# Kernel tuning notes

Measured on AMD Instinct MI355X. Metric: run time of the kernel, lower is better.

The kernel has to match this reference:

```python
import jax, jax.numpy as jnp
import numpy as np

TEMPERATURE = 0.5


def setup_inputs() -> dict:
    key = jax.random.key(0)
    k1, k2 = jax.random.split(key)
    N, D = 8192, 128
    features = jax.random.normal(k1, (N, D), dtype=jnp.float32)
    labels = jax.random.randint(k2, (N,), 0, 10, dtype=jnp.int64)
    return {"features": features, "labels": labels}


def reference(features, labels):
    # cosine similarity via normalized matmul (fused form of the broadcasted version)
    eps = 1e-8
    norm = jnp.maximum(jnp.linalg.norm(features, axis=-1, keepdims=True), eps)
    fn = features / norm
    sim = jnp.einsum('id,jd->ij', fn, fn) / TEMPERATURE  # [N, N]

    pos_mask = labels[:, None] == labels[None, :]        # [N, N] bool
    pos_f = pos_mask.astype(sim.dtype)
    neg_f = 1.0 - pos_f

    exp_pos = jnp.exp(sim * pos_f)                       # [N, N]
    exp_neg = jnp.sum(jnp.exp(sim * neg_f), axis=1, keepdims=True)  # [N, 1]

    loss_mat = -jnp.log(exp_pos / (exp_pos + exp_neg))   # [N, N]
    # mean over positive entries (jit-safe masked mean)
    num_pos = jnp.sum(pos_f)
    loss = jnp.sum(loss_mat * pos_f) / num_pos
    return loss
```

## Files before the change

kernel.cpp:

```cpp
#include <hip/hip_runtime.h>
#include <hip/hip_bf16.h>
#include <math.h>

#define NROWS 8192
#define DIM 128
#define BM 128
#define BN 128
#define CS 8
#define COLS_PER_SLAB (NROWS / CS)
#define CT_ITERS (COLS_PER_SLAB / BN)
#define RS (NROWS / BM)
#define SCALE 1.69864368f
#define LN2F 0.69314718056f

typedef __attribute__((ext_vector_type(8))) short bf16x8;
typedef __attribute__((ext_vector_type(4))) float f32x4;

__device__ __forceinline__ void gload16(const void* g, void* l) {
  __builtin_amdgcn_global_load_lds(
      (const __attribute__((address_space(1))) void*)g,
      (__attribute__((address_space(3))) void*)l, 16, 0, 0);
}

__device__ __forceinline__ void stage_tile(const ushort* __restrict__ fnb, int row0,
                                           char* tile, int w, int lane) {
  const char* gb = reinterpret_cast<const char*>(fnb);
#pragma unroll
  for (int i = 0; i < 8; ++i) {
    int rl = w * 32 + i * 4 + (lane >> 4);
    int src = ((lane & 15) ^ (rl & 7)) << 4;
    gload16(gb + (size_t)(row0 + rl) * 256 + src, tile + w * 8192 + i * 1024);
  }
}

__global__ __launch_bounds__(256) void k_norm(const float* __restrict__ f,
                                              __hip_bfloat16* __restrict__ fnb,
                                              float* __restrict__ losssum) {
  if (blockIdx.x == 0 && threadIdx.x == 0) losssum[0] = 0.f;
  int wave = threadIdx.x >> 6;
  int lane = threadIdx.x & 63;
  int row = blockIdx.x * 4 + wave;
  const float* src = f + (size_t)row * DIM;
  float v0 = src[lane];
  float v1 = src[lane + 64];
  float ss = v0 * v0 + v1 * v1;
#pragma unroll
  for (int o = 32; o > 0; o >>= 1) ss += __shfl_down(ss, o);
  ss = __shfl(ss, 0);
  float inv = SCALE / fmaxf(sqrtf(ss), 1e-8f);
  __hip_bfloat16* dst = fnb + (size_t)row * DIM;
  dst[lane] = __float2bfloat16(v0 * inv);
  dst[lane + 64] = __float2bfloat16(v1 * inv);
}

__global__ __launch_bounds__(256, 2) void k_main(
    const ushort* __restrict__ fnb, const int* __restrict__ lab,
    float* __restrict__ P) {
  __shared__ char lds[2 * BM * 256];
  const int t = threadIdx.x;
  const int lane = t & 63;
  const int w = t >> 6;
  const int wm = w >> 1, wn = w & 1;
  const int g = lane >> 4, li16 = lane & 15;
  const int cs = blockIdx.x;
  const int i0 = blockIdx.y * BM;
  const int jslab = cs * COLS_PER_SLAB;

  stage_tile(fnb, i0, lds, w, lane);
  stage_tile(fnb, jslab, lds + 32768, w, lane);
  asm volatile("s_waitcnt vmcnt(8)" ::: "memory");
  __builtin_amdgcn_s_barrier();

  bf16x8 af[4][4];
#pragma unroll
  for (int m = 0; m < 4; ++m) {
    int r = wm * 64 + m * 16 + li16;
#pragma unroll
    for (int ks = 0; ks < 4; ++ks) {
      int cb = ((ks * 4 + g) ^ (r & 7)) << 4;
      af[m][ks] = *reinterpret_cast<const bf16x8*>(lds + r * 256 + cb);
    }
  }
  asm volatile("s_waitcnt lgkmcnt(0)" ::: "memory");
  __builtin_amdgcn_sched_barrier(0);
  __builtin_amdgcn_s_barrier();

  int lr[4][4];
#pragma unroll
  for (int m = 0; m < 4; ++m)
#pragma unroll
    for (int r = 0; r < 4; ++r)
      lr[m][r] = lab[i0 + wm * 64 + m * 16 + g * 4 + r];

  float a_tot[4][4] = {}, a_pos[4][4] = {}, a_sim[4][4] = {};

#pragma unroll 1
  for (int ct = 0; ct < CT_ITERS; ++ct) {
    const int j0 = jslab + ct * BN;
    char* bufc = lds + ((size_t)((ct & 1) ^ 1) << 15);
    if (ct < CT_ITERS - 1)
      stage_tile(fnb, j0 + BN, lds + ((size_t)(ct & 1) << 15), w, lane);

    f32x4 acc[4][4];
#pragma unroll
    for (int m = 0; m < 4; ++m)
#pragma unroll
      for (int n = 0; n < 4; ++n) acc[m][n] = (f32x4){0.f, 0.f, 0.f, 0.f};

#pragma unroll
    for (int ks = 0; ks < 4; ++ks) {
      bf16x8 bf[4];
#pragma unroll
      for (int n = 0; n < 4; ++n) {
        int r = wn * 64 + n * 16 + li16;
        int cb = ((ks * 4 + g) ^ (r & 7)) << 4;
        bf[n] = *reinterpret_cast<const bf16x8*>(bufc + r * 256 + cb);
      }
#pragma unroll
      for (int m = 0; m < 4; ++m)
#pragma unroll
        for (int n = 0; n < 4; ++n)
          acc[m][n] = __builtin_amdgcn_mfma_f32_16x16x32_bf16(af[m][ks], bf[n], acc[m][n], 0, 0, 0);
    }

#pragma unroll
    for (int n = 0; n < 4; ++n) {
      const int lc = lab[j0 + wn * 64 + n * 16 + li16];
#pragma unroll
      for (int m = 0; m < 4; ++m)
#pragma unroll
        for (int r = 0; r < 4; ++r) {
          float u = acc[m][n][r];
          float E = __builtin_exp2f(u);
          float msk = (lr[m][r] == lc) ? 1.f : 0.f;
          a_tot[m][r] += E;
          a_pos[m][r] = fmaf(msk, E, a_pos[m][r]);
          a_sim[m][r] = fmaf(msk, u, a_sim[m][r]);
        }
    }

    asm volatile("s_waitcnt vmcnt(0)" ::: "memory");
    __builtin_amdgcn_s_barrier();
  }

#pragma unroll
  for (int m = 0; m < 4; ++m)
#pragma unroll
    for (int r = 0; r < 4; ++r)
#pragma unroll
      for (int off = 8; off > 0; off >>= 1) {
        a_tot[m][r] += __shfl_xor(a_tot[m][r], off);
        a_pos[m][r] += __shfl_xor(a_pos[m][r], off);
        a_sim[m][r] += __shfl_xor(a_sim[m][r], off);
      }

  __syncthreads();
  float* red = reinterpret_cast<float*>(lds);
  if (li16 == 0) {
#pragma unroll
    for (int m = 0; m < 4; ++m)
#pragma unroll
      for (int r = 0; r < 4; ++r) {
        int rl = wm * 64 + m * 16 + g * 4 + r;
        red[(rl * 2 + wn) * 3 + 0] = a_tot[m][r];
        red[(rl * 2 + wn) * 3 + 1] = a_pos[m][r];
        red[(rl * 2 + wn) * 3 + 2] = a_sim[m][r];
      }
  }
  __syncthreads();
  if (wn == 0 && li16 == 0) {
#pragma unroll
    for (int m = 0; m < 4; ++m)
#pragma unroll
      for (int r = 0; r < 4; ++r) {
        int rl = wm * 64 + m * 16 + g * 4 + r;
        float* dst = P + ((size_t)cs * NROWS + (i0 + rl)) * 3;
        dst[0] = red[(rl * 2) * 3 + 0] + red[(rl * 2 + 1) * 3 + 0];
        dst[1] = red[(rl * 2) * 3 + 1] + red[(rl * 2 + 1) * 3 + 1];
        dst[2] = red[(rl * 2) * 3 + 2] + red[(rl * 2 + 1) * 3 + 2];
      }
  }
}

__global__ __launch_bounds__(1024) void k_rowfinal(
    const float* __restrict__ P, const int* __restrict__ lab,
    float* __restrict__ losssum) {
  __shared__ int sh[16][16];
  __shared__ int hist_s[16];
  __shared__ float sred[1024];
  const int t = threadIdx.x;
  const int w = t >> 6;
  if ((t & 63) < 16) sh[w][t & 63] = 0;
  __syncthreads();
#pragma unroll
  for (int it = 0; it < NROWS / 1024; ++it)
    atomicAdd(&sh[w][lab[t + it * 1024]], 1);
  __syncthreads();
  if (t < 16) {
    int s = 0;
#pragma unroll
    for (int x = 0; x < 16; ++x) s += sh[x][t];
    hist_s[t] = s;
  }
  __syncthreads();

  int i = blockIdx.x * 1024 + t;
  float st = 0.f, sp = 0.f, sa = 0.f;
#pragma unroll
  for (int cs = 0; cs < CS; ++cs) {
    const float* p = P + ((size_t)cs * NROWS + i) * 3;
    st += p[0]; sp += p[1]; sa += p[2];
  }
  float cnt = (float)hist_s[lab[i]];
  float negtot = st - sp + cnt;
  float li = cnt * logf(negtot) + sp / negtot - LN2F * sa;
  sred[t] = li;
  __syncthreads();
  for (int s2 = 512; s2 > 0; s2 >>= 1) {
    if (t < s2) sred[t] += sred[t + s2];
    __syncthreads();
  }
  if (t == 0) {
    atomicAdd(&losssum[0], sred[0]);
    if (blockIdx.x == 0) {
      int np = 0;
#pragma unroll
      for (int c = 0; c < 10; ++c) np += hist_s[c] * hist_s[c];
      losssum[1] = (float)np;
    }
  }
}

__global__ void k_out(const float* __restrict__ losssum, float* __restrict__ out) {
  if (threadIdx.x == 0) out[0] = losssum[0] / losssum[1];
}

extern "C" void kernel_launch(void* const* d_in, const int* in_sizes, int n_in,
                              void* d_out, int out_size, void* d_ws, size_t ws_size,
                              hipStream_t stream) {
  const float* feat = (const float*)d_in[0];
  const int* lab = (const int*)d_in[1];
  float* out = (float*)d_out;
  char* ws = (char*)d_ws;

  __hip_bfloat16* fnb = (__hip_bfloat16*)ws;
  size_t off = (size_t)NROWS * DIM * 2;
  float* P = (float*)(ws + off); off += (size_t)CS * NROWS * 3 * 4;
  float* losssum = (float*)(ws + off);

  k_norm<<<NROWS / 4, 256, 0, stream>>>(feat, fnb, losssum);
  k_main<<<dim3(CS, RS), 256, 0, stream>>>((const ushort*)fnb, lab, P);
  k_rowfinal<<<NROWS / 1024, 1024, 0, stream>>>(P, lab, losssum);
  k_out<<<1, 64, 0, stream>>>(losssum, out);
}
```

Measured before the change: 62.45 us.

## Single-buffer LDS tile, load A fragments directly, double column slabs

The number of column slabs doubles, so the grid gets twice as many blocks, each covering half as many column tiles. The LDS B tile changes from double-buffered to single-buffered with synchronous staging between iterations, halving LDS per block. A fragments now come straight from global memory instead of through LDS, and the min-blocks hint in launch_bounds is dropped. The aim is more parallelism and occupancy, but the load of each next tile no longer overlaps compute and the partials buffer and final reduction grow.

```diff
diff --git a/kernel.cpp b/kernel.cpp
--- a/kernel.cpp
+++ b/kernel.cpp
@@ -6,7 +6,7 @@
 #define DIM 128
 #define BM 128
 #define BN 128
-#define CS 8
+#define CS 16
 #define COLS_PER_SLAB (NROWS / CS)
 #define CT_ITERS (COLS_PER_SLAB / BN)
 #define RS (NROWS / BM)
@@ -53,10 +53,10 @@
   dst[lane + 64] = __float2bfloat16(v1 * inv);
 }
 
-__global__ __launch_bounds__(256, 2) void k_main(
+__global__ __launch_bounds__(256) void k_main(
     const ushort* __restrict__ fnb, const int* __restrict__ lab,
     float* __restrict__ P) {
-  __shared__ char lds[2 * BM * 256];
+  __shared__ char lds[BM * 256];
   const int t = threadIdx.x;
   const int lane = t & 63;
   const int w = t >> 6;
@@ -66,24 +66,16 @@
   const int i0 = blockIdx.y * BM;
   const int jslab = cs * COLS_PER_SLAB;
 
-  stage_tile(fnb, i0, lds, w, lane);
-  stage_tile(fnb, jslab, lds + 32768, w, lane);
-  asm volatile("s_waitcnt vmcnt(8)" ::: "memory");
-  __builtin_amdgcn_s_barrier();
+  stage_tile(fnb, jslab, lds, w, lane);
 
   bf16x8 af[4][4];
 #pragma unroll
   for (int m = 0; m < 4; ++m) {
-    int r = wm * 64 + m * 16 + li16;
-#pragma unroll
-    for (int ks = 0; ks < 4; ++ks) {
-      int cb = ((ks * 4 + g) ^ (r & 7)) << 4;
-      af[m][ks] = *reinterpret_cast<const bf16x8*>(lds + r * 256 + cb);
-    }
-  }
-  asm volatile("s_waitcnt lgkmcnt(0)" ::: "memory");
-  __builtin_amdgcn_sched_barrier(0);
-  __builtin_amdgcn_s_barrier();
+    const ushort* arow = fnb + (size_t)(i0 + wm * 64 + m * 16 + li16) * DIM + g * 8;
+#pragma unroll
+    for (int ks = 0; ks < 4; ++ks)
+      af[m][ks] = *reinterpret_cast<const bf16x8*>(arow + ks * 32);
+  }
 
   int lr[4][4];
 #pragma unroll
@@ -93,13 +85,12 @@
       lr[m][r] = lab[i0 + wm * 64 + m * 16 + g * 4 + r];
 
   float a_tot[4][4] = {}, a_pos[4][4] = {}, a_sim[4][4] = {};
+
+  __syncthreads();
 
 #pragma unroll 1
   for (int ct = 0; ct < CT_ITERS; ++ct) {
     const int j0 = jslab + ct * BN;
-    char* bufc = lds + ((size_t)((ct & 1) ^ 1) << 15);
-    if (ct < CT_ITERS - 1)
-      stage_tile(fnb, j0 + BN, lds + ((size_t)(ct & 1) << 15), w, lane);
 
     f32x4 acc[4][4];
 #pragma unroll
@@ -114,7 +105,7 @@
       for (int n = 0; n < 4; ++n) {
         int r = wn * 64 + n * 16 + li16;
         int cb = ((ks * 4 + g) ^ (r & 7)) << 4;
-        bf[n] = *reinterpret_cast<const bf16x8*>(bufc + r * 256 + cb);
+        bf[n] = *reinterpret_cast<const bf16x8*>(lds + r * 256 + cb);
       }
 #pragma unroll
       for (int m = 0; m < 4; ++m)
@@ -139,8 +130,11 @@
         }
     }
 
-    asm volatile("s_waitcnt vmcnt(0)" ::: "memory");
-    __builtin_amdgcn_s_barrier();
+    if (ct < CT_ITERS - 1) {
+      __syncthreads();
+      stage_tile(fnb, j0 + BN, lds, w, lane);
+      __syncthreads();
+    }
   }
 
 #pragma unroll
```

Result: slower. 76.24 us (+22.1%).

## Split main tile across eight waves with narrower column tiles

Applied to the files above, without the earlier changes.

The similarity kernel now runs 512 threads per block as a 2x4 wave grid, and the column tile shrinks from 128 to 64. Each wave computes a 64x16 sub-tile per iteration instead of 64x64. A-operand fragments are re-read from LDS on every k-step rather than held in registers for the whole kernel. This cuts per-wave accumulator and fragment registers to allow more resident waves. In exchange it raises LDS read traffic, doubles the number of column iterations and barriers, and gives each wave less MFMA work per barrier.

```diff
diff --git a/kernel.cpp b/kernel.cpp
--- a/kernel.cpp
+++ b/kernel.cpp
@@ -5,7 +5,7 @@
 #define NROWS 8192
 #define DIM 128
 #define BM 128
-#define BN 128
+#define BN 64
 #define CS 8
 #define COLS_PER_SLAB (NROWS / CS)
 #define CT_ITERS (COLS_PER_SLAB / BN)
@@ -22,14 +22,25 @@
       (__attribute__((address_space(3))) void*)l, 16, 0, 0);
 }
 
-__device__ __forceinline__ void stage_tile(const ushort* __restrict__ fnb, int row0,
-                                           char* tile, int w, int lane) {
+__device__ __forceinline__ void stageA(const ushort* __restrict__ fnb, int row0,
+                                       char* tile, int w, int lane) {
   const char* gb = reinterpret_cast<const char*>(fnb);
 #pragma unroll
-  for (int i = 0; i < 8; ++i) {
-    int rl = w * 32 + i * 4 + (lane >> 4);
+  for (int i = 0; i < 4; ++i) {
+    int rl = w * 16 + i * 4 + (lane >> 4);
     int src = ((lane & 15) ^ (rl & 7)) << 4;
-    gload16(gb + (size_t)(row0 + rl) * 256 + src, tile + w * 8192 + i * 1024);
+    gload16(gb + (size_t)(row0 + rl) * 256 + src, tile + w * 4096 + i * 1024);
+  }
+}
+
+__device__ __forceinline__ void stageB(const ushort* __restrict__ fnb, int row0,
+                                       char* tile, int w, int lane) {
+  const char* gb = reinterpret_cast<const char*>(fnb);
+#pragma unroll
+  for (int i = 0; i < 2; ++i) {
+    int rl = w * 8 + i * 4 + (lane >> 4);
+    int src = ((lane & 15) ^ (rl & 7)) << 4;
+    gload16(gb + (size_t)(row0 + rl) * 256 + src, tile + w * 2048 + i * 1024);
   }
 }
 
@@ -53,37 +64,24 @@
   dst[lane + 64] = __float2bfloat16(v1 * inv);
 }
 
-__global__ __launch_bounds__(256, 2) void k_main(
+__global__ __launch_bounds__(512) void k_main(
     const ushort* __restrict__ fnb, const int* __restrict__ lab,
     float* __restrict__ P) {
-  __shared__ char lds[2 * BM * 256];
+  __shared__ char lds[65536];
+  char* Abase = lds;
+
   const int t = threadIdx.x;
   const int lane = t & 63;
   const int w = t >> 6;
-  const int wm = w >> 1, wn = w & 1;
+  const int wm = w >> 2;
+  const int wn = w & 3;
   const int g = lane >> 4, li16 = lane & 15;
   const int cs = blockIdx.x;
   const int i0 = blockIdx.y * BM;
   const int jslab = cs * COLS_PER_SLAB;
 
-  stage_tile(fnb, i0, lds, w, lane);
-  stage_tile(fnb, jslab, lds + 32768, w, lane);
-  asm volatile("s_waitcnt vmcnt(8)" ::: "memory");
-  __builtin_amdgcn_s_barrier();
-
-  bf16x8 af[4][4];
-#pragma unroll
-  for (int m = 0; m < 4; ++m) {
-    int r = wm * 64 + m * 16 + li16;
-#pragma unroll
-    for (int ks = 0; ks < 4; ++ks) {
-      int cb = ((ks * 4 + g) ^ (r & 7)) << 4;
-      af[m][ks] = *reinterpret_cast<const bf16x8*>(lds + r * 256 + cb);
-    }
-  }
-  asm volatile("s_waitcnt lgkmcnt(0)" ::: "memory");
-  __builtin_amdgcn_sched_barrier(0);
-  __builtin_amdgcn_s_barrier();
+  stageA(fnb, i0, Abase, w, lane);
+  stageB(fnb, jslab, lds + 32768, w, lane);
 
   int lr[4][4];
 #pragma unroll
@@ -93,51 +91,52 @@
       lr[m][r] = lab[i0 + wm * 64 + m * 16 + g * 4 + r];
 
   float a_tot[4][4] = {}, a_pos[4][4] = {}, a_sim[4][4] = {};
+
+  __syncthreads();
 
 #pragma unroll 1
   for (int ct = 0; ct < CT_ITERS; ++ct) {
     const int j0 = jslab + ct * BN;
-    char* bufc = lds + ((size_t)((ct & 1) ^ 1) << 15);
+    char* cur = lds + 32768 + ((ct & 1) << 14);
     if (ct < CT_ITERS - 1)
-      stage_tile(fnb, j0 + BN, lds + ((size_t)(ct & 1) << 15), w, lane);
-
-    f32x4 acc[4][4];
+      stageB(fnb, j0 + BN, lds + 32768 + (((ct + 1) & 1) << 14), w, lane);
+
+    f32x4 acc[4];
+#pragma unroll
+    for (int m = 0; m < 4; ++m) acc[m] = (f32x4){0.f, 0.f, 0.f, 0.f};
+
+#pragma unroll
+    for (int ks = 0; ks < 4; ++ks) {
+      bf16x8 bf;
+      {
+        int r2 = wn * 16 + li16;
+        int cb = ((ks * 4 + g) ^ (r2 & 7)) << 4;
+        bf = *reinterpret_cast<const bf16x8*>(cur + r2 * 256 + cb);
+      }
+      bf16x8 af[4];
+#pragma unroll
+      for (int m = 0; m < 4; ++m) {
+        int r = wm * 64 + m * 16 + li16;
+        int cb = ((ks * 4 + g) ^ (r & 7)) << 4;
+        af[m] = *reinterpret_cast<const bf16x8*>(Abase + r * 256 + cb);
+      }
+#pragma unroll
+      for (int m = 0; m < 4; ++m)
+        acc[m] = __builtin_amdgcn_mfma_f32_16x16x32_bf16(af[m], bf, acc[m], 0, 0, 0);
+    }
+
+    const int lc = lab[j0 + wn * 16 + li16];
 #pragma unroll
     for (int m = 0; m < 4; ++m)
 #pragma unroll
-      for (int n = 0; n < 4; ++n) acc[m][n] = (f32x4){0.f, 0.f, 0.f, 0.f};
-
-#pragma unroll
-    for (int ks = 0; ks < 4; ++ks) {
-      bf16x8 bf[4];
-#pragma unroll
-      for (int n = 0; n < 4; ++n) {
-        int r = wn * 64 + n * 16 + li16;
-        int cb = ((ks * 4 + g) ^ (r & 7)) << 4;
-        bf[n] = *reinterpret_cast<const bf16x8*>(bufc + r * 256 + cb);
-      }
-#pragma unroll
-      for (int m = 0; m < 4; ++m)
-#pragma unroll
-        for (int n = 0; n < 4; ++n)
-          acc[m][n] = __builtin_amdgcn_mfma_f32_16x16x32_bf16(af[m][ks], bf[n], acc[m][n], 0, 0, 0);
-    }
-
-#pragma unroll
-    for (int n = 0; n < 4; ++n) {
-      const int lc = lab[j0 + wn * 64 + n * 16 + li16];
-#pragma unroll
-      for (int m = 0; m < 4; ++m)
-#pragma unroll
-        for (int r = 0; r < 4; ++r) {
-          float u = acc[m][n][r];
-          float E = __builtin_exp2f(u);
-          float msk = (lr[m][r] == lc) ? 1.f : 0.f;
-          a_tot[m][r] += E;
-          a_pos[m][r] = fmaf(msk, E, a_pos[m][r]);
-          a_sim[m][r] = fmaf(msk, u, a_sim[m][r]);
-        }
-    }
+      for (int r = 0; r < 4; ++r) {
+        float u = acc[m][r];
+        float E = __builtin_exp2f(u);
+        float msk = (lr[m][r] == lc) ? 1.f : 0.f;
+        a_tot[m][r] += E;
+        a_pos[m][r] = fmaf(msk, E, a_pos[m][r]);
+        a_sim[m][r] = fmaf(msk, u, a_sim[m][r]);
+      }
 
     asm volatile("s_waitcnt vmcnt(0)" ::: "memory");
     __builtin_amdgcn_s_barrier();
@@ -155,16 +154,16 @@
       }
 
   __syncthreads();
-  float* red = reinterpret_cast<float*>(lds);
+  float(*red)[4][3] = reinterpret_cast<float(*)[4][3]>(lds);
   if (li16 == 0) {
 #pragma unroll
     for (int m = 0; m < 4; ++m)
 #pragma unroll
       for (int r = 0; r < 4; ++r) {
         int rl = wm * 64 + m * 16 + g * 4 + r;
-        red[(rl * 2 + wn) * 3 + 0] = a_tot[m][r];
-        red[(rl * 2 + wn) * 3 + 1] = a_pos[m][r];
-        red[(rl * 2 + wn) * 3 + 2] = a_sim[m][r];
+        red[rl][wn][0] = a_tot[m][r];
+        red[rl][wn][1] = a_pos[m][r];
+        red[rl][wn][2] = a_sim[m][r];
       }
   }
   __syncthreads();
@@ -175,9 +174,9 @@
       for (int r = 0; r < 4; ++r) {
         int rl = wm * 64 + m * 16 + g * 4 + r;
         float* dst = P + ((size_t)cs * NROWS + (i0 + rl)) * 3;
-        dst[0] = red[(rl * 2) * 3 + 0] + red[(rl * 2 + 1) * 3 + 0];
-        dst[1] = red[(rl * 2) * 3 + 1] + red[(rl * 2 + 1) * 3 + 1];
-        dst[2] = red[(rl * 2) * 3 + 2] + red[(rl * 2 + 1) * 3 + 2];
+        dst[0] = red[rl][0][0] + red[rl][1][0] + red[rl][2][0] + red[rl][3][0];
+        dst[1] = red[rl][0][1] + red[rl][1][1] + red[rl][2][1] + red[rl][3][1];
+        dst[2] = red[rl][0][2] + red[rl][1][2] + red[rl][2][2] + red[rl][3][2];
       }
   }
 }
@@ -249,7 +248,7 @@
   float* losssum = (float*)(ws + off);
 
   k_norm<<<NROWS / 4, 256, 0, stream>>>(feat, fnb, losssum);
-  k_main<<<dim3(CS, RS), 256, 0, stream>>>((const ushort*)fnb, lab, P);
+  k_main<<<dim3(CS, RS), 512, 0, stream>>>((const ushort*)fnb, lab, P);
   k_rowfinal<<<NROWS / 1024, 1024, 0, stream>>>(P, lab, losssum);
   k_out<<<1, 64, 0, stream>>>(losssum, out);
 }
```

Result: faster. 59.97 us (-4.0%).
